# Optimization experiments

Hardware: AMD Instinct MI355X
Metric: run time of the kernel (lower is better)

Reference implementation:

```python
import jax, jax.numpy as jnp
import numpy as np


def _mlp(x, W1, b1, W2, b2, W3, b3):
    # flatten -> fc(784,512) -> relu -> fc(512,128) -> relu -> fc(128,C)
    h = x.reshape(x.shape[0], -1)
    h = jax.nn.relu(h @ W1.T + b1)
    h = jax.nn.relu(h @ W2.T + b2)
    return h @ W3.T + b3


def setup_inputs() -> dict:
    key = jax.random.key(0)
    ks = jax.random.split(key, 6)
    B, Bu, C, D = 65536, 4096, 10, 28 * 28
    return {
        "x": jax.random.uniform(ks[0], (B, 28, 28), jnp.float32),
        "y": jax.random.randint(ks[1], (B,), 0, C),
        "x_unlab": jax.random.uniform(ks[2], (Bu, 28, 28), jnp.float32),
        "W1": jax.random.normal(ks[3], (512, D), jnp.float32) * 0.03,
        "b1": jnp.zeros((512,), jnp.float32),
        "W2": jax.random.normal(ks[4], (128, 512), jnp.float32) * 0.05,
        "b2": jnp.zeros((128,), jnp.float32),
        "W3": jax.random.normal(ks[5], (C, 128), jnp.float32) * 0.08,
        "b3": jnp.zeros((C,), jnp.float32),
    }


def reference(x, y, x_unlab, W1, b1, W2, b2, W3, b3):
    n_classes = W3.shape[0]
    # ---- labeled branch: BCEWithLogitsLoss(mean) vs one-hot targets ----
    logits = _mlp(x, W1, b1, W2, b2, W3, b3)  # [B, C]
    t = jax.nn.one_hot(y, n_classes, dtype=logits.dtype)
    bce = jnp.mean(jnp.maximum(logits, 0.0) - logits * t
                   + jnp.log1p(jnp.exp(-jnp.abs(logits))))
    # ---- unlabeled branch: semantic loss ----
    # sem_loss(probs): s[c] = sum_i p_i[c] * prod_{j != i} (1 - p_j[c]);
    # return mean over classes of -log(s). Done in log domain with a single
    # O(Bu) leave-one-out sum instead of the original O(Bu^2) double loop.
    o_u = _mlp(x_unlab, W1, b1, W2, b2, W3, b3)       # [Bu, C]
    logp = jax.nn.log_sigmoid(o_u)                     # log p
    log1mp = jax.nn.log_sigmoid(-o_u)                  # log (1 - p)
    loo = jnp.sum(log1mp, axis=0, keepdims=True) - log1mp  # leave-one-out log-prod
    log_s = jax.scipy.special.logsumexp(logp + loo, axis=0)  # [C]
    sl = jnp.mean(-log_s)
    # compute_loss returns (bce, sl); stacked here as a length-2 vector
    return jnp.stack([bce, sl])
```

## Files before the change

### kernel.cpp

```cpp
#include <hip/hip_runtime.h>
#include <hip/hip_bf16.h>
#include <stdint.h>

typedef unsigned short ushort_t;
typedef __bf16 bf16x8 __attribute__((ext_vector_type(8)));
typedef float f32x4 __attribute__((ext_vector_type(4)));

__device__ __forceinline__ ushort_t f2bf(float f) {
    union { float f; unsigned u; } v; v.f = f;
    unsigned u = v.u;
    unsigned r = u + 0x7fffu + ((u >> 16) & 1u);
    return (ushort_t)(r >> 16);
}
__device__ __forceinline__ float bf2f(ushort_t h) {
    union { unsigned u; float f; } v; v.u = ((unsigned)h) << 16;
    return v.f;
}

#define GLDS16(gsrc, ldst)                                                    \
    __builtin_amdgcn_global_load_lds(                                         \
        (const __attribute__((address_space(1))) void*)(gsrc),                \
        (__attribute__((address_space(3))) void*)(ldst), 16, 0, 0)

__global__ __launch_bounds__(256) void prep_kernel(
    const float* __restrict__ W1, const float* __restrict__ W2,
    ushort_t* __restrict__ W1p, ushort_t* __restrict__ W2b,
    float* __restrict__ stats)
{
    int idx = blockIdx.x * 256 + threadIdx.x;
    if (idx < 512 * 800) {
        int n = idx / 800, k = idx - n * 800;
        W1p[idx] = (k < 784) ? f2bf(W1[n * 784 + k]) : (ushort_t)0;
    }
    if (idx < 128 * 512) W2b[idx] = f2bf(W2[idx]);
    if (idx == 0) stats[0] = 0.0f;
}

__global__ __launch_bounds__(256) void xconvert_kernel(
    const float* __restrict__ x, const float* __restrict__ xu,
    ushort_t* __restrict__ Xb)
{
    int idx = blockIdx.x * 256 + threadIdx.x;
    int r = idx / 50, c = idx - r * 50;
    uint4 lo, hi;
    if (c < 49) {
        const float* src = (r < 65536) ? (x + (size_t)r * 784)
                                       : (xu + (size_t)(r - 65536) * 784);
        const float4* p = (const float4*)(src + c * 16);
        float4 f0 = p[0], f1 = p[1], f2 = p[2], f3 = p[3];
        lo.x = ((unsigned)f2bf(f0.y) << 16) | f2bf(f0.x);
        lo.y = ((unsigned)f2bf(f0.w) << 16) | f2bf(f0.z);
        lo.z = ((unsigned)f2bf(f1.y) << 16) | f2bf(f1.x);
        lo.w = ((unsigned)f2bf(f1.w) << 16) | f2bf(f1.z);
        hi.x = ((unsigned)f2bf(f2.y) << 16) | f2bf(f2.x);
        hi.y = ((unsigned)f2bf(f2.w) << 16) | f2bf(f2.z);
        hi.z = ((unsigned)f2bf(f3.y) << 16) | f2bf(f3.x);
        hi.w = ((unsigned)f2bf(f3.w) << 16) | f2bf(f3.z);
    } else {
        lo = make_uint4(0, 0, 0, 0);
        hi = make_uint4(0, 0, 0, 0);
    }
    uint4* dst = (uint4*)(Xb + (size_t)r * 800 + c * 16);
    dst[0] = lo;
    dst[1] = hi;
}

__global__ __launch_bounds__(256) void gemm1_kernel(
    const ushort_t* __restrict__ Xb, const ushort_t* __restrict__ W1p,
    const float* __restrict__ b1, ushort_t* __restrict__ h1)
{
    __shared__ ushort_t As[128 * 32];
    __shared__ ushort_t Bs[128 * 32];

    const int b = blockIdx.x;
    const int xcd = b & 7, s = b >> 3;
    const int tile_n = s & 3;
    const int tile_m = xcd * 68 + (s >> 2);

    const int tid = threadIdx.x;
    const int w = tid >> 6, lane = tid & 63;
    const int wm = w >> 1, wn = w & 1;
    const int quad = lane >> 4, lc = lane & 15;
    const int row_in = lane >> 2;
    const int koff = (lane & 3) * 8;

    f32x4 acc[4][4];
#pragma unroll
    for (int i = 0; i < 4; i++)
#pragma unroll
        for (int j = 0; j < 4; j++)
#pragma unroll
            for (int r = 0; r < 4; r++) acc[i][j][r] = 0.0f;

    for (int k0 = 0; k0 < 800; k0 += 32) {
#pragma unroll
        for (int c = 0; c < 2; c++) {
            int row = (w * 2 + c) * 16 + row_in;
            const ushort_t* srcA =
                Xb + (size_t)(tile_m * 128 + row) * 800 + k0 + koff;
            GLDS16(srcA, As + (w * 2 + c) * 512);
            const ushort_t* srcB =
                W1p + (size_t)(tile_n * 128 + row) * 800 + k0 + koff;
            GLDS16(srcB, Bs + (w * 2 + c) * 512);
        }
        __syncthreads();

        bf16x8 af[4], bfr[4];
#pragma unroll
        for (int i = 0; i < 4; i++)
            af[i] = *(const bf16x8*)&As[(wm * 64 + i * 16 + lc) * 32 + quad * 8];
#pragma unroll
        for (int j = 0; j < 4; j++)
            bfr[j] = *(const bf16x8*)&Bs[(wn * 64 + j * 16 + lc) * 32 + quad * 8];
#pragma unroll
        for (int i = 0; i < 4; i++)
#pragma unroll
            for (int j = 0; j < 4; j++)
                acc[i][j] = __builtin_amdgcn_mfma_f32_16x16x32_bf16(
                    af[i], bfr[j], acc[i][j], 0, 0, 0);
        __syncthreads();
    }

    float bias[4];
#pragma unroll
    for (int j = 0; j < 4; j++)
        bias[j] = b1[tile_n * 128 + wn * 64 + j * 16 + lc];
#pragma unroll
    for (int i = 0; i < 4; i++) {
        int gr0 = tile_m * 128 + wm * 64 + i * 16 + quad * 4;
#pragma unroll
        for (int j = 0; j < 4; j++) {
            int gc = tile_n * 128 + wn * 64 + j * 16 + lc;
#pragma unroll
            for (int r = 0; r < 4; r++) {
                float v = acc[i][j][r] + bias[j];
                v = fmaxf(v, 0.0f);
                h1[(size_t)(gr0 + r) * 512 + gc] = f2bf(v);
            }
        }
    }
}

__global__ __launch_bounds__(256) void gemm1_inline_kernel(
    const float* __restrict__ x, const float* __restrict__ xu,
    const ushort_t* __restrict__ W1p, const float* __restrict__ b1,
    ushort_t* __restrict__ h1)
{
    __shared__ ushort_t As[128 * 32];
    __shared__ ushort_t Bs[128 * 32];

    const int tile_n = blockIdx.x & 3;
    const int tile_m = blockIdx.x >> 2;
    const int tid = threadIdx.x;
    const int w = tid >> 6, lane = tid & 63;
    const int wm = w >> 1, wn = w & 1;
    const int quad = lane >> 4, lc = lane & 15;

    const int arow = tid >> 1;
    const int akoff = (tid & 1) * 16;
    const int grow = tile_m * 128 + arow;
    const float* asrc = (grow < 65536) ? (x + (size_t)grow * 784)
                                       : (xu + (size_t)(grow - 65536) * 784);
    const int brow_in = (lane >> 2);
    const int bkoff = (lane & 3) * 8;

    f32x4 acc[4][4];
#pragma unroll
    for (int i = 0; i < 4; i++)
#pragma unroll
        for (int j = 0; j < 4; j++)
#pragma unroll
            for (int r = 0; r < 4; r++) acc[i][j][r] = 0.0f;

    for (int k0 = 0; k0 < 800; k0 += 32) {
#pragma unroll
        for (int c = 0; c < 2; c++) {
            int row = (w * 2 + c) * 16 + brow_in;
            const ushort_t* src =
                W1p + (size_t)(tile_n * 128 + row) * 800 + k0 + bkoff;
            GLDS16(src, Bs + (w * 2 + c) * 512);
        }
        {
            int kch = k0 + akoff;
            uint4 lo, hi;
            if (kch < 784) {
                const float4* p = (const float4*)(asrc + kch);
                float4 f0 = p[0], f1 = p[1], f2 = p[2], f3 = p[3];
                lo.x = ((unsigned)f2bf(f0.y) << 16) | f2bf(f0.x);
                lo.y = ((unsigned)f2bf(f0.w) << 16) | f2bf(f0.z);
                lo.z = ((unsigned)f2bf(f1.y) << 16) | f2bf(f1.x);
                lo.w = ((unsigned)f2bf(f1.w) << 16) | f2bf(f1.z);
                hi.x = ((unsigned)f2bf(f2.y) << 16) | f2bf(f2.x);
                hi.y = ((unsigned)f2bf(f2.w) << 16) | f2bf(f2.z);
                hi.z = ((unsigned)f2bf(f3.y) << 16) | f2bf(f3.x);
                hi.w = ((unsigned)f2bf(f3.w) << 16) | f2bf(f3.z);
            } else {
                lo = make_uint4(0, 0, 0, 0);
                hi = make_uint4(0, 0, 0, 0);
            }
            *(uint4*)&As[arow * 32 + akoff] = lo;
            *(uint4*)&As[arow * 32 + akoff + 8] = hi;
        }
        __syncthreads();

        bf16x8 af[4], bfr[4];
#pragma unroll
        for (int i = 0; i < 4; i++)
            af[i] = *(const bf16x8*)&As[(wm * 64 + i * 16 + lc) * 32 + quad * 8];
#pragma unroll
        for (int j = 0; j < 4; j++)
            bfr[j] = *(const bf16x8*)&Bs[(wn * 64 + j * 16 + lc) * 32 + quad * 8];
#pragma unroll
        for (int i = 0; i < 4; i++)
#pragma unroll
            for (int j = 0; j < 4; j++)
                acc[i][j] = __builtin_amdgcn_mfma_f32_16x16x32_bf16(
                    af[i], bfr[j], acc[i][j], 0, 0, 0);
        __syncthreads();
    }

    float bias[4];
#pragma unroll
    for (int j = 0; j < 4; j++)
        bias[j] = b1[tile_n * 128 + wn * 64 + j * 16 + lc];
#pragma unroll
    for (int i = 0; i < 4; i++) {
        int gr0 = tile_m * 128 + wm * 64 + i * 16 + quad * 4;
#pragma unroll
        for (int j = 0; j < 4; j++) {
            int gc = tile_n * 128 + wn * 64 + j * 16 + lc;
#pragma unroll
            for (int r = 0; r < 4; r++) {
                float v = acc[i][j][r] + bias[j];
                v = fmaxf(v, 0.0f);
                h1[(size_t)(gr0 + r) * 512 + gc] = f2bf(v);
            }
        }
    }
}

__global__ __launch_bounds__(256) void gemm2_kernel(
    const ushort_t* __restrict__ h1, const ushort_t* __restrict__ W2b,
    const float* __restrict__ b2, ushort_t* __restrict__ h2)
{
    __shared__ ushort_t As[64 * 32];
    __shared__ ushort_t Bs[128 * 32];

    const int tile_m = blockIdx.x;
    const int tid = threadIdx.x;
    const int w = tid >> 6, lane = tid & 63;
    const int wm = w >> 1, wn = w & 1;
    const int quad = lane >> 4, lc = lane & 15;
    const int row_in = lane >> 2;
    const int koff = (lane & 3) * 8;

    f32x4 acc[2][4];
#pragma unroll
    for (int i = 0; i < 2; i++)
#pragma unroll
        for (int j = 0; j < 4; j++)
#pragma unroll
            for (int r = 0; r < 4; r++) acc[i][j][r] = 0.0f;

    for (int k0 = 0; k0 < 512; k0 += 32) {
        {
            int row = w * 16 + row_in;
            const ushort_t* srcA =
                h1 + (size_t)(tile_m * 64 + row) * 512 + k0 + koff;
            GLDS16(srcA, As + w * 512);
        }
#pragma unroll
        for (int c = 0; c < 2; c++) {
            int row = (w * 2 + c) * 16 + row_in;
            const ushort_t* srcB = W2b + (size_t)row * 512 + k0 + koff;
            GLDS16(srcB, Bs + (w * 2 + c) * 512);
        }
        __syncthreads();

        bf16x8 af[2], bfr[4];
#pragma unroll
        for (int i = 0; i < 2; i++)
            af[i] = *(const bf16x8*)&As[(wm * 32 + i * 16 + lc) * 32 + quad * 8];
#pragma unroll
        for (int j = 0; j < 4; j++)
            bfr[j] = *(const bf16x8*)&Bs[(wn * 64 + j * 16 + lc) * 32 + quad * 8];
#pragma unroll
        for (int i = 0; i < 2; i++)
#pragma unroll
            for (int j = 0; j < 4; j++)
                acc[i][j] = __builtin_amdgcn_mfma_f32_16x16x32_bf16(
                    af[i], bfr[j], acc[i][j], 0, 0, 0);
        __syncthreads();
    }

    float bias[4];
#pragma unroll
    for (int j = 0; j < 4; j++) bias[j] = b2[wn * 64 + j * 16 + lc];
#pragma unroll
    for (int i = 0; i < 2; i++) {
        int gr0 = tile_m * 64 + wm * 32 + i * 16 + quad * 4;
#pragma unroll
        for (int j = 0; j < 4; j++) {
            int gc = wn * 64 + j * 16 + lc;
#pragma unroll
            for (int r = 0; r < 4; r++) {
                float v = acc[i][j][r] + bias[j];
                v = fmaxf(v, 0.0f);
                h2[(size_t)(gr0 + r) * 128 + gc] = f2bf(v);
            }
        }
    }
}

__global__ __launch_bounds__(256) void loss_kernel(
    const ushort_t* __restrict__ h2, const int* __restrict__ y,
    const float* __restrict__ W3, const float* __restrict__ b3,
    float* __restrict__ stats, float* __restrict__ logits_u)
{
    __shared__ float W3s[10 * 128];
    __shared__ float b3s[10];
    __shared__ ushort_t h2s[64 * 128];
    __shared__ float red[4];

    const int tid = threadIdx.x;
    for (int i = tid; i < 1280; i += 256) W3s[i] = W3[i];
    if (tid < 10) b3s[tid] = b3[tid];

    const size_t row0 = (size_t)blockIdx.x * 64;
    const ushort_t* src = h2 + row0 * 128;
#pragma unroll
    for (int i = tid * 8; i < 64 * 128; i += 256 * 8)
        *(uint4*)&h2s[i] = *(const uint4*)&src[i];
    __syncthreads();

    float bce_part = 0.0f;
    for (int o = tid; o < 640; o += 256) {
        int r = o / 10, c = o - r * 10;
        size_t grow = row0 + r;
        float acc = b3s[c];
        const ushort_t* hr = &h2s[r * 128];
        const float* wr = &W3s[c * 128];
#pragma unroll 8
        for (int k = 0; k < 128; k++) acc += bf2f(hr[k]) * wr[k];
        if (grow < 65536) {
            float t = (y[grow] == c) ? 1.0f : 0.0f;
            bce_part += fmaxf(acc, 0.0f) - acc * t +
                        log1pf(__expf(-fabsf(acc)));
        } else {
            logits_u[(grow - 65536) * 10 + c] = acc;
        }
    }
#pragma unroll
    for (int s = 32; s > 0; s >>= 1) bce_part += __shfl_down(bce_part, s, 64);
    if ((tid & 63) == 0) red[tid >> 6] = bce_part;
    __syncthreads();
    if (tid == 0) {
        float v = red[0] + red[1] + red[2] + red[3];
        atomicAdd(stats, v);
    }
}

__global__ __launch_bounds__(640) void finisher_kernel(
    const float* __restrict__ logits_u, const float* __restrict__ stats,
    float* __restrict__ out)
{
    __shared__ float Rs[64][10];
    __shared__ float Rm[64][10];
    __shared__ float Scol[10], Mcol[10];

    const int tid = threadIdx.x;
    const int g = tid / 10, c = tid - g * 10;
    float s = 0.0f, m = -1e30f;
    for (int i = g; i < 4096; i += 64) {
        float o = logits_u[i * 10 + c];
        s += fminf(-o, 0.0f) - log1pf(__expf(-fabsf(o)));
        m = fmaxf(m, o);
    }
    Rs[g][c] = s;
    Rm[g][c] = m;
    __syncthreads();
    if (tid < 10) {
        float ss = 0.0f, mm = -1e30f;
        for (int gg = 0; gg < 64; gg++) {
            ss += Rs[gg][tid];
            mm = fmaxf(mm, Rm[gg][tid]);
        }
        Scol[tid] = ss;
        Mcol[tid] = mm;
    }
    __syncthreads();
    float e = 0.0f;
    float mm = Mcol[c];
    for (int i = g; i < 4096; i += 64)
        e += __expf(logits_u[i * 10 + c] - mm);
    Rs[g][c] = e;
    __syncthreads();
    if (tid == 0) {
        float sl = 0.0f;
        for (int cc = 0; cc < 10; cc++) {
            float ee = 0.0f;
            for (int gg = 0; gg < 64; gg++) ee += Rs[gg][cc];
            sl += -(Scol[cc] + Mcol[cc] + __logf(ee));
        }
        sl *= 0.1f;
        out[0] = stats[0] * (1.0f / (65536.0f * 10.0f));
        out[1] = sl;
    }
}

extern "C" void kernel_launch(void* const* d_in, const int* in_sizes, int n_in,
                              void* d_out, int out_size, void* d_ws,
                              size_t ws_size, hipStream_t stream)
{
    const float* x  = (const float*)d_in[0];
    const int*   y  = (const int*)d_in[1];
    const float* xu = (const float*)d_in[2];
    const float* W1 = (const float*)d_in[3];
    const float* b1 = (const float*)d_in[4];
    const float* W2 = (const float*)d_in[5];
    const float* b2 = (const float*)d_in[6];
    const float* W3 = (const float*)d_in[7];
    const float* b3 = (const float*)d_in[8];
    float* out = (float*)d_out;

    char* ws = (char*)d_ws;
    ushort_t* W1p      = (ushort_t*)(ws + 0);
    ushort_t* W2b      = (ushort_t*)(ws + 819200);
    float*    stats    = (float*)(ws + 950272);
    float*    logits_u = (float*)(ws + 950528);
    ushort_t* h1       = (ushort_t*)(ws + 1114368);
    ushort_t* h2       = (ushort_t*)(ws + 72417536);
    ushort_t* Xb       = (ushort_t*)(ws + 72417536);
    const size_t FAST_WS_NEED = 183828736;

    prep_kernel<<<1600, 256, 0, stream>>>(W1, W2, W1p, W2b, stats);
    if (ws_size >= FAST_WS_NEED) {
        xconvert_kernel<<<13600, 256, 0, stream>>>(x, xu, Xb);
        gemm1_kernel<<<2176, 256, 0, stream>>>(Xb, W1p, b1, h1);
    } else {
        gemm1_inline_kernel<<<2176, 256, 0, stream>>>(x, xu, W1p, b1, h1);
    }
    gemm2_kernel<<<1088, 256, 0, stream>>>(h1, W2b, b2, h2);
    loss_kernel<<<1088, 256, 0, stream>>>(h2, y, W3, b3, stats, logits_u);
    finisher_kernel<<<1, 640, 0, stream>>>(logits_u, stats, out);
    (void)in_sizes; (void)n_in; (void)out_size; (void)ws_size;
}
```

Measured before the change: 552.9 us.

## Fuse fp32→bf16 conversion into GEMM1 and fuse GEMM2 with loss

```diff
diff --git a/kernel.cpp b/kernel.cpp
--- a/kernel.cpp
+++ b/kernel.cpp
@@ -36,41 +36,13 @@
     if (idx == 0) stats[0] = 0.0f;
 }
 
-__global__ __launch_bounds__(256) void xconvert_kernel(
+__global__ __launch_bounds__(256) void gemm1f_kernel(
     const float* __restrict__ x, const float* __restrict__ xu,
-    ushort_t* __restrict__ Xb)
-{
-    int idx = blockIdx.x * 256 + threadIdx.x;
-    int r = idx / 50, c = idx - r * 50;
-    uint4 lo, hi;
-    if (c < 49) {
-        const float* src = (r < 65536) ? (x + (size_t)r * 784)
-                                       : (xu + (size_t)(r - 65536) * 784);
-        const float4* p = (const float4*)(src + c * 16);
-        float4 f0 = p[0], f1 = p[1], f2 = p[2], f3 = p[3];
-        lo.x = ((unsigned)f2bf(f0.y) << 16) | f2bf(f0.x);
-        lo.y = ((unsigned)f2bf(f0.w) << 16) | f2bf(f0.z);
-        lo.z = ((unsigned)f2bf(f1.y) << 16) | f2bf(f1.x);
-        lo.w = ((unsigned)f2bf(f1.w) << 16) | f2bf(f1.z);
-        hi.x = ((unsigned)f2bf(f2.y) << 16) | f2bf(f2.x);
-        hi.y = ((unsigned)f2bf(f2.w) << 16) | f2bf(f2.z);
-        hi.z = ((unsigned)f2bf(f3.y) << 16) | f2bf(f3.x);
-        hi.w = ((unsigned)f2bf(f3.w) << 16) | f2bf(f3.z);
-    } else {
-        lo = make_uint4(0, 0, 0, 0);
-        hi = make_uint4(0, 0, 0, 0);
-    }
-    uint4* dst = (uint4*)(Xb + (size_t)r * 800 + c * 16);
-    dst[0] = lo;
-    dst[1] = hi;
-}
-
-__global__ __launch_bounds__(256) void gemm1_kernel(
-    const ushort_t* __restrict__ Xb, const ushort_t* __restrict__ W1p,
-    const float* __restrict__ b1, ushort_t* __restrict__ h1)
-{
-    __shared__ ushort_t As[128 * 32];
-    __shared__ ushort_t Bs[128 * 32];
+    const ushort_t* __restrict__ W1p, const float* __restrict__ b1,
+    ushort_t* __restrict__ h1)
+{
+    __shared__ ushort_t As[2][128 * 32];
+    __shared__ ushort_t Bs[2][128 * 32];
 
     const int b = blockIdx.x;
     const int xcd = b & 7, s = b >> 3;
@@ -84,85 +56,13 @@
     const int row_in = lane >> 2;
     const int koff = (lane & 3) * 8;
 
-    f32x4 acc[4][4];
-#pragma unroll
-    for (int i = 0; i < 4; i++)
-#pragma unroll
-        for (int j = 0; j < 4; j++)
-#pragma unroll
-            for (int r = 0; r < 4; r++) acc[i][j][r] = 0.0f;
-
-    for (int k0 = 0; k0 < 800; k0 += 32) {
-#pragma unroll
-        for (int c = 0; c < 2; c++) {
-            int row = (w * 2 + c) * 16 + row_in;
-            const ushort_t* srcA =
-                Xb + (size_t)(tile_m * 128 + row) * 800 + k0 + koff;
-            GLDS16(srcA, As + (w * 2 + c) * 512);
-            const ushort_t* srcB =
-                W1p + (size_t)(tile_n * 128 + row) * 800 + k0 + koff;
-            GLDS16(srcB, Bs + (w * 2 + c) * 512);
-        }
-        __syncthreads();
-
-        bf16x8 af[4], bfr[4];
-#pragma unroll
-        for (int i = 0; i < 4; i++)
-            af[i] = *(const bf16x8*)&As[(wm * 64 + i * 16 + lc) * 32 + quad * 8];
-#pragma unroll
-        for (int j = 0; j < 4; j++)
-            bfr[j] = *(const bf16x8*)&Bs[(wn * 64 + j * 16 + lc) * 32 + quad * 8];
-#pragma unroll
-        for (int i = 0; i < 4; i++)
-#pragma unroll
-            for (int j = 0; j < 4; j++)
-                acc[i][j] = __builtin_amdgcn_mfma_f32_16x16x32_bf16(
-                    af[i], bfr[j], acc[i][j], 0, 0, 0);
-        __syncthreads();
-    }
-
-    float bias[4];
-#pragma unroll
-    for (int j = 0; j < 4; j++)
-        bias[j] = b1[tile_n * 128 + wn * 64 + j * 16 + lc];
-#pragma unroll
-    for (int i = 0; i < 4; i++) {
-        int gr0 = tile_m * 128 + wm * 64 + i * 16 + quad * 4;
-#pragma unroll
-        for (int j = 0; j < 4; j++) {
-            int gc = tile_n * 128 + wn * 64 + j * 16 + lc;
-#pragma unroll
-            for (int r = 0; r < 4; r++) {
-                float v = acc[i][j][r] + bias[j];
-                v = fmaxf(v, 0.0f);
-                h1[(size_t)(gr0 + r) * 512 + gc] = f2bf(v);
-            }
-        }
-    }
-}
-
-__global__ __launch_bounds__(256) void gemm1_inline_kernel(
-    const float* __restrict__ x, const float* __restrict__ xu,
-    const ushort_t* __restrict__ W1p, const float* __restrict__ b1,
-    ushort_t* __restrict__ h1)
-{
-    __shared__ ushort_t As[128 * 32];
-    __shared__ ushort_t Bs[128 * 32];
-
-    const int tile_n = blockIdx.x & 3;
-    const int tile_m = blockIdx.x >> 2;
-    const int tid = threadIdx.x;
-    const int w = tid >> 6, lane = tid & 63;
-    const int wm = w >> 1, wn = w & 1;
-    const int quad = lane >> 4, lc = lane & 15;
-
     const int arow = tid >> 1;
     const int akoff = (tid & 1) * 16;
     const int grow = tile_m * 128 + arow;
     const float* asrc = (grow < 65536) ? (x + (size_t)grow * 784)
                                        : (xu + (size_t)(grow - 65536) * 784);
-    const int brow_in = (lane >> 2);
-    const int bkoff = (lane & 3) * 8;
+    ushort_t* adst0 = &As[0][arow * 32 + akoff];
+    ushort_t* adst1 = &As[1][arow * 32 + akoff];
 
     f32x4 acc[4][4];
 #pragma unroll
@@ -172,50 +72,115 @@
 #pragma unroll
             for (int r = 0; r < 4; r++) acc[i][j][r] = 0.0f;
 
-    for (int k0 = 0; k0 < 800; k0 += 32) {
+    float4 p0a, p0b, p0c, p0d, p1a, p1b, p1c, p1d;
+    {
+        const float4* q0 = (const float4*)(asrc + akoff);
+        p0a = q0[0]; p0b = q0[1]; p0c = q0[2]; p0d = q0[3];
+        const float4* q1 = (const float4*)(asrc + 32 + akoff);
+        p1a = q1[0]; p1b = q1[1]; p1c = q1[2]; p1d = q1[3];
+    }
+
+    for (int k0 = 0; k0 < 800; k0 += 64) {
+        const bool has2 = (k0 + 32) < 800;
+
 #pragma unroll
         for (int c = 0; c < 2; c++) {
-            int row = (w * 2 + c) * 16 + brow_in;
-            const ushort_t* src =
-                W1p + (size_t)(tile_n * 128 + row) * 800 + k0 + bkoff;
-            GLDS16(src, Bs + (w * 2 + c) * 512);
-        }
+            int row = (w * 2 + c) * 16 + row_in;
+            const ushort_t* srcB =
+                W1p + (size_t)(tile_n * 128 + row) * 800 + k0 + koff;
+            GLDS16(srcB, &Bs[0][(w * 2 + c) * 512]);
+        }
+        if (has2) {
+#pragma unroll
+            for (int c = 0; c < 2; c++) {
+                int row = (w * 2 + c) * 16 + row_in;
+                const ushort_t* srcB =
+                    W1p + (size_t)(tile_n * 128 + row) * 800 + k0 + 32 + koff;
+                GLDS16(srcB, &Bs[1][(w * 2 + c) * 512]);
+            }
+        }
+
         {
-            int kch = k0 + akoff;
             uint4 lo, hi;
-            if (kch < 784) {
-                const float4* p = (const float4*)(asrc + kch);
-                float4 f0 = p[0], f1 = p[1], f2 = p[2], f3 = p[3];
-                lo.x = ((unsigned)f2bf(f0.y) << 16) | f2bf(f0.x);
-                lo.y = ((unsigned)f2bf(f0.w) << 16) | f2bf(f0.z);
-                lo.z = ((unsigned)f2bf(f1.y) << 16) | f2bf(f1.x);
-                lo.w = ((unsigned)f2bf(f1.w) << 16) | f2bf(f1.z);
-                hi.x = ((unsigned)f2bf(f2.y) << 16) | f2bf(f2.x);
-                hi.y = ((unsigned)f2bf(f2.w) << 16) | f2bf(f2.z);
-                hi.z = ((unsigned)f2bf(f3.y) << 16) | f2bf(f3.x);
-                hi.w = ((unsigned)f2bf(f3.w) << 16) | f2bf(f3.z);
+            if (k0 + akoff <= 768) {
+                lo.x = ((unsigned)f2bf(p0a.y) << 16) | f2bf(p0a.x);
+                lo.y = ((unsigned)f2bf(p0a.w) << 16) | f2bf(p0a.z);
+                lo.z = ((unsigned)f2bf(p0b.y) << 16) | f2bf(p0b.x);
+                lo.w = ((unsigned)f2bf(p0b.w) << 16) | f2bf(p0b.z);
+                hi.x = ((unsigned)f2bf(p0c.y) << 16) | f2bf(p0c.x);
+                hi.y = ((unsigned)f2bf(p0c.w) << 16) | f2bf(p0c.z);
+                hi.z = ((unsigned)f2bf(p0d.y) << 16) | f2bf(p0d.x);
+                hi.w = ((unsigned)f2bf(p0d.w) << 16) | f2bf(p0d.z);
             } else {
                 lo = make_uint4(0, 0, 0, 0);
                 hi = make_uint4(0, 0, 0, 0);
             }
-            *(uint4*)&As[arow * 32 + akoff] = lo;
-            *(uint4*)&As[arow * 32 + akoff + 8] = hi;
+            *(uint4*)adst0 = lo;
+            *(uint4*)(adst0 + 8) = hi;
+        }
+        if (has2) {
+            uint4 lo, hi;
+            if (k0 + 32 + akoff <= 768) {
+                lo.x = ((unsigned)f2bf(p1a.y) << 16) | f2bf(p1a.x);
+                lo.y = ((unsigned)f2bf(p1a.w) << 16) | f2bf(p1a.z);
+                lo.z = ((unsigned)f2bf(p1b.y) << 16) | f2bf(p1b.x);
+                lo.w = ((unsigned)f2bf(p1b.w) << 16) | f2bf(p1b.z);
+                hi.x = ((unsigned)f2bf(p1c.y) << 16) | f2bf(p1c.x);
+                hi.y = ((unsigned)f2bf(p1c.w) << 16) | f2bf(p1c.z);
+                hi.z = ((unsigned)f2bf(p1d.y) << 16) | f2bf(p1d.x);
+                hi.w = ((unsigned)f2bf(p1d.w) << 16) | f2bf(p1d.z);
+            } else {
+                lo = make_uint4(0, 0, 0, 0);
+                hi = make_uint4(0, 0, 0, 0);
+            }
+            *(uint4*)adst1 = lo;
+            *(uint4*)(adst1 + 8) = hi;
+        }
+
+        {
+            int kn0 = k0 + 64 + akoff;
+            if (kn0 <= 768) {
+                const float4* q = (const float4*)(asrc + kn0);
+                p0a = q[0]; p0b = q[1]; p0c = q[2]; p0d = q[3];
+            }
+            int kn1 = k0 + 96 + akoff;
+            if (kn1 <= 768) {
+                const float4* q = (const float4*)(asrc + kn1);
+                p1a = q[0]; p1b = q[1]; p1c = q[2]; p1d = q[3];
+            }
         }
         __syncthreads();
 
-        bf16x8 af[4], bfr[4];
-#pragma unroll
-        for (int i = 0; i < 4; i++)
-            af[i] = *(const bf16x8*)&As[(wm * 64 + i * 16 + lc) * 32 + quad * 8];
-#pragma unroll
-        for (int j = 0; j < 4; j++)
-            bfr[j] = *(const bf16x8*)&Bs[(wn * 64 + j * 16 + lc) * 32 + quad * 8];
-#pragma unroll
-        for (int i = 0; i < 4; i++)
+        {
+            bf16x8 af[4], bfr[4];
+#pragma unroll
+            for (int i = 0; i < 4; i++)
+                af[i] = *(const bf16x8*)&As[0][(wm * 64 + i * 16 + lc) * 32 + quad * 8];
 #pragma unroll
             for (int j = 0; j < 4; j++)
-                acc[i][j] = __builtin_amdgcn_mfma_f32_16x16x32_bf16(
-                    af[i], bfr[j], acc[i][j], 0, 0, 0);
+                bfr[j] = *(const bf16x8*)&Bs[0][(wn * 64 + j * 16 + lc) * 32 + quad * 8];
+#pragma unroll
+            for (int i = 0; i < 4; i++)
+#pragma unroll
+                for (int j = 0; j < 4; j++)
+                    acc[i][j] = __builtin_amdgcn_mfma_f32_16x16x32_bf16(
+                        af[i], bfr[j], acc[i][j], 0, 0, 0);
+        }
+        if (has2) {
+            bf16x8 af[4], bfr[4];
+#pragma unroll
+            for (int i = 0; i < 4; i++)
+                af[i] = *(const bf16x8*)&As[1][(wm * 64 + i * 16 + lc) * 32 + quad * 8];
+#pragma unroll
+            for (int j = 0; j < 4; j++)
+                bfr[j] = *(const bf16x8*)&Bs[1][(wn * 64 + j * 16 + lc) * 32 + quad * 8];
+#pragma unroll
+            for (int i = 0; i < 4; i++)
+#pragma unroll
+                for (int j = 0; j < 4; j++)
+                    acc[i][j] = __builtin_amdgcn_mfma_f32_16x16x32_bf16(
+                        af[i], bfr[j], acc[i][j], 0, 0, 0);
+        }
         __syncthreads();
     }
 
@@ -239,125 +204,115 @@
     }
 }
 
-__global__ __launch_bounds__(256) void gemm2_kernel(
+__global__ __launch_bounds__(256) void gemm23_kernel(
     const ushort_t* __restrict__ h1, const ushort_t* __restrict__ W2b,
-    const float* __restrict__ b2, ushort_t* __restrict__ h2)
-{
-    __shared__ ushort_t As[64 * 32];
-    __shared__ ushort_t Bs[128 * 32];
-
-    const int tile_m = blockIdx.x;
+    const float* __restrict__ b2, const int* __restrict__ y,
+    const float* __restrict__ W3, const float* __restrict__ b3,
+    float* __restrict__ stats, float* __restrict__ logits_u)
+{
+    __shared__ ushort_t As[2][64 * 32];
+    __shared__ ushort_t Bs[2][128 * 32];
+    __shared__ float W3s[1280];
+    __shared__ float b3s[10];
+    __shared__ float red[4];
+
     const int tid = threadIdx.x;
     const int w = tid >> 6, lane = tid & 63;
     const int wm = w >> 1, wn = w & 1;
     const int quad = lane >> 4, lc = lane & 15;
     const int row_in = lane >> 2;
     const int koff = (lane & 3) * 8;
-
-    f32x4 acc[2][4];
-#pragma unroll
-    for (int i = 0; i < 2; i++)
-#pragma unroll
-        for (int j = 0; j < 4; j++)
-#pragma unroll
-            for (int r = 0; r < 4; r++) acc[i][j][r] = 0.0f;
-
-    for (int k0 = 0; k0 < 512; k0 += 32) {
-        {
-            int row = w * 16 + row_in;
-            const ushort_t* srcA =
-                h1 + (size_t)(tile_m * 64 + row) * 512 + k0 + koff;
-            GLDS16(srcA, As + w * 512);
-        }
-#pragma unroll
-        for (int c = 0; c < 2; c++) {
-            int row = (w * 2 + c) * 16 + row_in;
-            const ushort_t* srcB = W2b + (size_t)row * 512 + k0 + koff;
-            GLDS16(srcB, Bs + (w * 2 + c) * 512);
-        }
-        __syncthreads();
-
-        bf16x8 af[2], bfr[4];
-#pragma unroll
-        for (int i = 0; i < 2; i++)
-            af[i] = *(const bf16x8*)&As[(wm * 32 + i * 16 + lc) * 32 + quad * 8];
-#pragma unroll
-        for (int j = 0; j < 4; j++)
-            bfr[j] = *(const bf16x8*)&Bs[(wn * 64 + j * 16 + lc) * 32 + quad * 8];
-#pragma unroll
-        for (int i = 0; i < 2; i++)
-#pragma unroll
-            for (int j = 0; j < 4; j++)
-                acc[i][j] = __builtin_amdgcn_mfma_f32_16x16x32_bf16(
-                    af[i], bfr[j], acc[i][j], 0, 0, 0);
-        __syncthreads();
-    }
-
-    float bias[4];
-#pragma unroll
-    for (int j = 0; j < 4; j++) bias[j] = b2[wn * 64 + j * 16 + lc];
-#pragma unroll
-    for (int i = 0; i < 2; i++) {
-        int gr0 = tile_m * 64 + wm * 32 + i * 16 + quad * 4;
-#pragma unroll
-        for (int j = 0; j < 4; j++) {
-            int gc = wn * 64 + j * 16 + lc;
-#pragma unroll
-            for (int r = 0; r < 4; r++) {
-                float v = acc[i][j][r] + bias[j];
-                v = fmaxf(v, 0.0f);
-                h2[(size_t)(gr0 + r) * 128 + gc] = f2bf(v);
-            }
-        }
-    }
-}
-
-__global__ __launch_bounds__(256) void loss_kernel(
-    const ushort_t* __restrict__ h2, const int* __restrict__ y,
-    const float* __restrict__ W3, const float* __restrict__ b3,
-    float* __restrict__ stats, float* __restrict__ logits_u)
-{
-    __shared__ float W3s[10 * 128];
-    __shared__ float b3s[10];
-    __shared__ ushort_t h2s[64 * 128];
-    __shared__ float red[4];
-
-    const int tid = threadIdx.x;
+    const int tile_m = blockIdx.x;
+
     for (int i = tid; i < 1280; i += 256) W3s[i] = W3[i];
     if (tid < 10) b3s[tid] = b3[tid];
 
-    const size_t row0 = (size_t)blockIdx.x * 64;
-    const ushort_t* src = h2 + row0 * 128;
-#pragma unroll
-    for (int i = tid * 8; i < 64 * 128; i += 256 * 8)
-        *(uint4*)&h2s[i] = *(const uint4*)&src[i];
-    __syncthreads();
-
+    f32x4 acc[2][4];
+#pragma unroll
+    for (int i = 0; i < 2; i++)
+#pragma unroll
+        for (int j = 0; j < 4; j++)
+#pragma unroll
+            for (int r = 0; r < 4; r++) acc[i][j][r] = 0.0f;
+
+    for (int k0 = 0; k0 < 512; k0 += 64) {
+#pragma unroll
+        for (int p = 0; p < 2; p++) {
+            {
+                int rowA = w * 16 + row_in;
+                const ushort_t* srcA =
+                    h1 + (size_t)(tile_m * 64 + rowA) * 512 + k0 + p * 32 + koff;
+                GLDS16(srcA, &As[p][w * 512]);
+            }
+#pragma unroll
+            for (int c = 0; c < 2; c++) {
+                int rowB = (w * 2 + c) * 16 + row_in;
+                const ushort_t* srcB =
+                    W2b + (size_t)rowB * 512 + k0 + p * 32 + koff;
+                GLDS16(srcB, &Bs[p][(w * 2 + c) * 512]);
+            }
+        }
+        __syncthreads();
+#pragma unroll
+        for (int p = 0; p < 2; p++) {
+            bf16x8 af[2], bfr[4];
+#pragma unroll
+            for (int i = 0; i < 2; i++)
+                af[i] = *(const bf16x8*)&As[p][(wm * 32 + i * 16 + lc) * 32 + quad * 8];
+#pragma unroll
+            for (int j = 0; j < 4; j++)
+                bfr[j] = *(const bf16x8*)&Bs[p][(wn * 64 + j * 16 + lc) * 32 + quad * 8];
+#pragma unroll
+            for (int i = 0; i < 2; i++)
+#pragma unroll
+                for (int j = 0; j < 4; j++)
+                    acc[i][j] = __builtin_amdgcn_mfma_f32_16x16x32_bf16(
+                        af[i], bfr[j], acc[i][j], 0, 0, 0);
+        }
+        __syncthreads();
+    }
+
+    ushort_t* h2s = &Bs[0][0];
+    float bias[4];
+#pragma unroll
+    for (int j = 0; j < 4; j++) bias[j] = b2[wn * 64 + j * 16 + lc];
+#pragma unroll
+    for (int i = 0; i < 2; i++) {
+        int row0 = wm * 32 + i * 16 + quad * 4;
+#pragma unroll
+        for (int j = 0; j < 4; j++) {
+            int col = wn * 64 + j * 16 + lc;
+#pragma unroll
+            for (int r = 0; r < 4; r++) {
+                float v = fmaxf(acc[i][j][r] + bias[j], 0.0f);
+                h2s[(row0 + r) * 128 + col] = f2bf(v);
+            }
+        }
+    }
+    __syncthreads();
+
+    const size_t row0g = (size_t)tile_m * 64;
     float bce_part = 0.0f;
     for (int o = tid; o < 640; o += 256) {
         int r = o / 10, c = o - r * 10;
-        size_t grow = row0 + r;
-        float acc = b3s[c];
+        size_t grw = row0g + r;
+        float a = b3s[c];
         const ushort_t* hr = &h2s[r * 128];
         const float* wr = &W3s[c * 128];
 #pragma unroll 8
-        for (int k = 0; k < 128; k++) acc += bf2f(hr[k]) * wr[k];
-        if (grow < 65536) {
-            float t = (y[grow] == c) ? 1.0f : 0.0f;
-            bce_part += fmaxf(acc, 0.0f) - acc * t +
-                        log1pf(__expf(-fabsf(acc)));
+        for (int k = 0; k < 128; k++) a += bf2f(hr[k]) * wr[k];
+        if (grw < 65536) {
+            float t = (y[grw] == c) ? 1.0f : 0.0f;
+            bce_part += fmaxf(a, 0.0f) - a * t + log1pf(__expf(-fabsf(a)));
         } else {
-            logits_u[(grow - 65536) * 10 + c] = acc;
+            logits_u[(grw - 65536) * 10 + c] = a;
         }
     }
 #pragma unroll
     for (int s = 32; s > 0; s >>= 1) bce_part += __shfl_down(bce_part, s, 64);
     if ((tid & 63) == 0) red[tid >> 6] = bce_part;
     __syncthreads();
-    if (tid == 0) {
-        float v = red[0] + red[1] + red[2] + red[3];
-        atomicAdd(stats, v);
-    }
+    if (tid == 0) atomicAdd(stats, red[0] + red[1] + red[2] + red[3]);
 }
 
 __global__ __launch_bounds__(640) void finisher_kernel(
@@ -429,19 +384,11 @@
     float*    stats    = (float*)(ws + 950272);
     float*    logits_u = (float*)(ws + 950528);
     ushort_t* h1       = (ushort_t*)(ws + 1114368);
-    ushort_t* h2       = (ushort_t*)(ws + 72417536);
-    ushort_t* Xb       = (ushort_t*)(ws + 72417536);
-    const size_t FAST_WS_NEED = 183828736;
 
     prep_kernel<<<1600, 256, 0, stream>>>(W1, W2, W1p, W2b, stats);
-    if (ws_size >= FAST_WS_NEED) {
-        xconvert_kernel<<<13600, 256, 0, stream>>>(x, xu, Xb);
-        gemm1_kernel<<<2176, 256, 0, stream>>>(Xb, W1p, b1, h1);
-    } else {
-        gemm1_inline_kernel<<<2176, 256, 0, stream>>>(x, xu, W1p, b1, h1);
-    }
-    gemm2_kernel<<<1088, 256, 0, stream>>>(h1, W2b, b2, h2);
-    loss_kernel<<<1088, 256, 0, stream>>>(h2, y, W3, b3, stats, logits_u);
+    gemm1f_kernel<<<2176, 256, 0, stream>>>(x, xu, W1p, b1, h1);
+    gemm23_kernel<<<1088, 256, 0, stream>>>(h1, W2b, b2, y, W3, b3, stats,
+                                            logits_u);
     finisher_kernel<<<1, 640, 0, stream>>>(logits_u, stats, out);
     (void)in_sizes; (void)n_in; (void)out_size; (void)ws_size;
 }
```

Measured after the change: 503.3 us. 1.1x faster.
